# Optimization experiments

Hardware: AMD Instinct MI355X
Metric: run time of the kernel (lower is better)

## Reference

```python
import jax, jax.numpy as jnp
import numpy as np
from jax import lax

B, C_IN, C_OUT, KK, KS = 8, 32, 64, 4, 3
D, H, W = 32, 64, 64
PAD = 1

def setup_inputs() -> dict:
    key = jax.random.key(0)
    ks = jax.random.split(key, 12)
    s = 0.02
    return {
        "x": jax.random.normal(ks[0], (B, C_IN, D, H, W), jnp.float32),
        # K candidate conv kernels and biases
        "weight": jax.random.normal(ks[1], (KK, C_OUT, C_IN, KS, KS, KS), jnp.float32) * s,
        "cbias": jnp.zeros((KK, C_OUT), jnp.float32),
        "temperature": jnp.float32(34.0),
        # attention key path: BN(affine, eval-mode) -> GELU -> 1x1 conv (linear)
        "bn1_g": jnp.ones((C_IN,), jnp.float32),
        "bn1_b": jnp.zeros((C_IN,), jnp.float32),
        "w1": jax.random.normal(ks[2], (C_IN, C_IN), jnp.float32) * s,
        "b1": jnp.zeros((C_IN,), jnp.float32),
        "bn2_g": jnp.ones((C_IN,), jnp.float32),
        "bn2_b": jnp.zeros((C_IN,), jnp.float32),
        "w2": jax.random.normal(ks[3], (C_IN, C_IN), jnp.float32) * s,
        "b2": jnp.zeros((C_IN,), jnp.float32),
        "bn3_g": jnp.ones((C_IN,), jnp.float32),
        "bn3_b": jnp.zeros((C_IN,), jnp.float32),
        "w3": jax.random.normal(ks[4], (KK, C_IN), jnp.float32) * s,
        "b3": jnp.zeros((KK,), jnp.float32),
    }

def _attention(p, temperature, bn1_g, bn1_b, w1, b1, bn2_g, bn2_b, w2, b2, bn3_g, bn3_b, w3, b3):
    # p: [B, C] pooled features. 1x1x1 convs on 1x1x1 maps == linear layers.
    gelu = lambda t: jax.nn.gelu(t, approximate=False)  # torch nn.GELU default is erf
    a = gelu(p * bn1_g + bn1_b)          # BN (eval: rm=0, rv=1) + GELU
    a = a @ w1.T + b1
    a = gelu(a * bn2_g + bn2_b)
    a = a @ w2.T + b2
    a = a + p                            # ResidualLayer (plain add)
    a = a * bn3_g + bn3_b
    logits = a @ w3.T + b3               # [B, K]
    return jax.nn.softmax(logits / temperature, axis=1)

def reference(x, weight, cbias, temperature, bn1_g, bn1_b, w1, b1,
              bn2_g, bn2_b, w2, b2, bn3_g, bn3_b, w3, b3):
    # x: [B, C_in, D, H, W]
    p = x.mean(axis=(2, 3, 4))  # AdaptiveAvgPool3d(1)
    attn = _attention(p, temperature, bn1_g, bn1_b, w1, b1,
                      bn2_g, bn2_b, w2, b2, bn3_g, bn3_b, w3, b3)  # [B, K]
    # per-sample aggregated kernels / bias
    agg_w = jnp.einsum('bk,koidhw->boidhw', attn, weight)  # [B, O, I, k, k, k]
    agg_b = attn @ cbias                                    # [B, O]
    # grouped-conv trick (groups=B) == per-sample conv3d -> vmap over batch
    def conv1(xi, wi):
        return lax.conv_general_dilated(
            xi[None], wi, window_strides=(1, 1, 1),
            padding=[(PAD, PAD)] * 3,
            dimension_numbers=('NCDHW', 'OIDHW', 'NCDHW'))[0]
    out = jax.vmap(conv1)(x, agg_w)  # [B, O, D, H, W]
    return out + agg_b[:, :, None, None, None]
```

## Files before the change

kernel.cpp:

```cpp
#include <hip/hip_runtime.h>
#include <hip/hip_bf16.h>
#include <math.h>

#define B_   8
#define CIN  32
#define COUT 64
#define KK_  4
#define DD   32
#define HH   64
#define WW   64
#define HW   (HH*WW)
#define DHW  (DD*HH*WW)

typedef __attribute__((ext_vector_type(8)))  short bf16x8;
typedef __attribute__((ext_vector_type(16))) float f32x16;

__device__ __forceinline__ unsigned short f2bf(float f) {
    union { float f; unsigned int u; } v; v.f = f;
    return (unsigned short)((v.u + 0x7FFFu + ((v.u >> 16) & 1u)) >> 16);
}
__device__ __forceinline__ void gll16(const void* g, void* l) {
    __builtin_amdgcn_global_load_lds(
        (const __attribute__((address_space(1))) void*)g,
        (__attribute__((address_space(3))) void*)l, 16, 0, 0);
}

__global__ __launch_bounds__(256) void transpose_kernel(const float* __restrict__ x,
                                                        unsigned short* __restrict__ xt,
                                                        float* __restrict__ pblk) {
    const int t = threadIdx.x;
    const int r = t >> 6, w = t & 63;
    const int hb = blockIdx.x;
    const int h = (hb << 2) + r;
    const int d = blockIdx.y, b = blockIdx.z;

    const float* xb = x + (size_t)b*CIN*DHW + (size_t)d*HW + (size_t)h*WW + w;
    float f[CIN];
    #pragma unroll
    for (int c = 0; c < CIN; ++c) f[c] = xb[(size_t)c * DHW];

    unsigned int packed[CIN/2];
    #pragma unroll
    for (int c2 = 0; c2 < CIN/2; ++c2) {
        unsigned int lo = f2bf(f[2*c2]);
        unsigned int hi = f2bf(f[2*c2+1]);
        packed[c2] = lo | (hi << 16);
    }
    char* row = (char*)xt + (size_t)((b*DD + d)*HH + h) * 4096;
    #pragma unroll
    for (int q = 0; q < 4; ++q) {
        uint4 v = make_uint4(packed[4*q], packed[4*q+1], packed[4*q+2], packed[4*q+3]);
        *(uint4*)(row + q*1024 + (((w << 4)) ^ (q << 4))) = v;
    }

    #pragma unroll
    for (int off = 32; off > 0; off >>= 1) {
        #pragma unroll
        for (int c = 0; c < CIN; ++c) f[c] += __shfl_xor(f[c], off);
    }
    __shared__ float ws4[4][CIN];
    if ((t & 63) < CIN) ws4[r][t & 63] = f[t & 63];
    __syncthreads();
    if (t < CIN)
        pblk[(size_t)((b*DD + d)*16 + hb)*CIN + t] =
            ws4[0][t] + ws4[1][t] + ws4[2][t] + ws4[3][t];
}

__device__ __forceinline__ float gelu_erf(float v) {
    return 0.5f * v * (1.f + erff(v * 0.70710678118654752f));
}

__global__ void attn_kernel(const float* __restrict__ pblk,
                            const float* __restrict__ temperature,
                            const float* __restrict__ bn1_g, const float* __restrict__ bn1_b,
                            const float* __restrict__ w1,    const float* __restrict__ b1,
                            const float* __restrict__ bn2_g, const float* __restrict__ bn2_b,
                            const float* __restrict__ w2,    const float* __restrict__ b2,
                            const float* __restrict__ bn3_g, const float* __restrict__ bn3_b,
                            const float* __restrict__ w3,    const float* __restrict__ b3,
                            const float* __restrict__ cbias,
                            float* __restrict__ attn_out, float* __restrict__ aggb_out) {
    __shared__ float A[B_][CIN], A2[B_][CIN];
    __shared__ float L[B_][KK_], ATT[B_][KK_];
    const int t = threadIdx.x;
    const int b = t >> 5, c = t & 31;

    float pv = 0.f;
    for (int i = 0; i < DD*16; ++i) pv += pblk[(size_t)(b*DD*16 + i)*CIN + c];
    pv *= (1.f / (float)DHW);

    A[b][c] = gelu_erf(pv * bn1_g[c] + bn1_b[c]);
    __syncthreads();

    float s = b1[c];
    for (int j = 0; j < CIN; ++j) s += A[b][j] * w1[c*CIN + j];
    A2[b][c] = gelu_erf(s * bn2_g[c] + bn2_b[c]);
    __syncthreads();

    float s2 = b2[c];
    for (int j = 0; j < CIN; ++j) s2 += A2[b][j] * w2[c*CIN + j];
    s2 += pv;
    s2 = s2 * bn3_g[c] + bn3_b[c];
    __syncthreads();
    A[b][c] = s2;
    __syncthreads();

    if (c < KK_) {
        float lv = b3[c];
        for (int j = 0; j < CIN; ++j) lv += A[b][j] * w3[c*CIN + j];
        L[b][c] = lv;
    }
    __syncthreads();

    const float T = temperature[0];
    if (c < KK_) {
        float m = fmaxf(fmaxf(L[b][0], L[b][1]), fmaxf(L[b][2], L[b][3]));
        float e = expf((L[b][c] - m) / T);
        float den = 0.f;
        for (int j = 0; j < KK_; ++j) den += expf((L[b][j] - m) / T);
        float av = e / den;
        ATT[b][c] = av;
        attn_out[b*KK_ + c] = av;
    }
    __syncthreads();

    for (int o = c; o < COUT; o += CIN) {
        float sb = 0.f;
        for (int k = 0; k < KK_; ++k) sb += ATT[b][k] * cbias[k*COUT + o];
        aggb_out[b*COUT + o] = sb;
    }
}

__global__ void aggw_kernel(const float* __restrict__ weight,
                            const float* __restrict__ attn,
                            unsigned short* __restrict__ wt) {
    const int idx = blockIdx.x * 256 + threadIdx.x;
    const int ci   = idx & 31;
    const int co   = (idx >> 5) & 63;
    int r          = idx >> 11;
    const int kpos = r % 27;
    const int b    = r / 27;
    float s = 0.f;
    #pragma unroll
    for (int k = 0; k < KK_; ++k)
        s += attn[b*KK_ + k] * weight[((k*COUT + co)*CIN + ci)*27 + kpos];
    wt[idx] = f2bf(s);
}

__global__ __launch_bounds__(128, 1) void conv_mfma(const unsigned short* __restrict__ xt,
                                                    const unsigned short* __restrict__ wt,
                                                    const float* __restrict__ aggb,
                                                    float* __restrict__ out) {
    __shared__ char smem[19 * 4096];
    const int t    = threadIdx.x;
    const int lane = t & 63;
    const int wv   = t >> 6;
    const int lw   = lane & 31, lh = lane >> 5;

    const int id = blockIdx.x;
    const int b  = id & 7;
    const int h  = (id >> 3) & 63;
    const int d0 = ((id >> 9) & 7) << 2;

    const char* xb  = (const char*)xt + (size_t)(b*DD)*HH*4096;
    const char* wtb = (const char*)wt + (size_t)b * 27 * 4096;

    *(uint4*)&smem[18*4096 + t*32]      = make_uint4(0u,0u,0u,0u);
    *(uint4*)&smem[18*4096 + t*32 + 16] = make_uint4(0u,0u,0u,0u);

    for (int rid = wv; rid < 18; rid += 2) {
        const int j = rid / 3, ho = rid % 3;
        const int zd = d0 - 1 + j, yh = h - 1 + ho;
        char* dst = smem + (size_t)(rid << 12);
        if ((unsigned)zd < DD && (unsigned)yh < HH) {
            const char* src = xb + (size_t)(zd*HH + yh)*4096 + lane*16;
            #pragma unroll
            for (int q = 0; q < 4; ++q) gll16(src + (q << 10), dst + (q << 10));
        } else {
            #pragma unroll
            for (int q = 0; q < 4; ++q)
                *(uint4*)(dst + (q << 10) + lane*16) = make_uint4(0u,0u,0u,0u);
        }
    }
    __syncthreads();

    f32x16 acc[2][4];
    #pragma unroll
    for (int cb = 0; cb < 2; ++cb)
        #pragma unroll
        for (int r = 0; r < 4; ++r)
            acc[cb][r] = (f32x16){};

    const int a_off = lw*64 + lh*16;
    const int o0 = lh, o1 = 2 + lh;

    bf16x8 av[2][12];
    bf16x8 bc[2][12];

    auto loadA = [&](int p, int par) {
        const int kh = p / 3, kw = p % 3;
        #pragma unroll
        for (int kd = 0; kd < 3; ++kd) {
            const char* wk = wtb + (size_t)(((kd*3 + kh)*3 + kw) << 12);
            av[par][kd*4+0] = *(const bf16x8*)(wk + a_off);
            av[par][kd*4+1] = *(const bf16x8*)(wk + 32 + a_off);
            av[par][kd*4+2] = *(const bf16x8*)(wk + 2048 + a_off);
            av[par][kd*4+3] = *(const bf16x8*)(wk + 2048 + 32 + a_off);
        }
    };
    auto loadB = [&](int p, int par) {
        const int kh = p / 3, kw = p % 3;
        const int wp  = (wv << 5) + lw + kw - 1;
        const bool oob = ((unsigned)wp >= (unsigned)WW);
        const int wpc = oob ? lw : wp;
        const int sw0 = (o0 << 10) + ((wpc << 4) ^ (o0 << 4));
        const int sw1 = (o1 << 10) + ((wpc << 4) ^ (o1 << 4));
        #pragma unroll
        for (int j = 0; j < 6; ++j) {
            const int rb = oob ? 18*4096 : ((j*3 + kh) << 12);
            bc[par][j*2+0] = *(const bf16x8*)&smem[rb + sw0];
            bc[par][j*2+1] = *(const bf16x8*)&smem[rb + sw1];
        }
    };

    loadA(0, 0);
    loadB(0, 0);

    #pragma unroll
    for (int p = 0; p < 9; ++p) {
        const int cur = p & 1, nxt = cur ^ 1;
        if (p < 8) { loadA(p + 1, nxt); loadB(p + 1, nxt); }
        __builtin_amdgcn_sched_barrier(0);
        __builtin_amdgcn_s_setprio(1);
        #pragma unroll
        for (int kd = 0; kd < 3; ++kd) {
            #pragma unroll
            for (int r = 0; r < 4; ++r) {
                const int j = r + kd;
                acc[0][r] = __builtin_amdgcn_mfma_f32_32x32x16_bf16(av[cur][kd*4+0], bc[cur][j*2+0], acc[0][r], 0, 0, 0);
                acc[0][r] = __builtin_amdgcn_mfma_f32_32x32x16_bf16(av[cur][kd*4+1], bc[cur][j*2+1], acc[0][r], 0, 0, 0);
                acc[1][r] = __builtin_amdgcn_mfma_f32_32x32x16_bf16(av[cur][kd*4+2], bc[cur][j*2+0], acc[1][r], 0, 0, 0);
                acc[1][r] = __builtin_amdgcn_mfma_f32_32x32x16_bf16(av[cur][kd*4+3], bc[cur][j*2+1], acc[1][r], 0, 0, 0);
            }
        }
        __builtin_amdgcn_s_setprio(0);
    }

    const float* ab = aggb + b*COUT;
    const int sp0 = h*WW + (wv << 5) + lw;
    #pragma unroll
    for (int cb = 0; cb < 2; ++cb) {
        #pragma unroll
        for (int reg = 0; reg < 16; ++reg) {
            const int co = (cb << 5) + (reg & 3) + ((reg >> 2) << 3) + (lh << 2);
            const float bb = ab[co];
            float* oc = out + ((size_t)(b*COUT + co))*DHW + sp0;
            #pragma unroll
            for (int r = 0; r < 4; ++r)
                oc[(size_t)(d0 + r)*HW] = acc[cb][r][reg] + bb;
        }
    }
}

extern "C" void kernel_launch(void* const* d_in, const int* in_sizes, int n_in,
                              void* d_out, int out_size, void* d_ws, size_t ws_size,
                              hipStream_t stream) {
    const float* x           = (const float*)d_in[0];
    const float* weight      = (const float*)d_in[1];
    const float* cbias       = (const float*)d_in[2];
    const float* temperature = (const float*)d_in[3];
    const float* bn1_g       = (const float*)d_in[4];
    const float* bn1_b       = (const float*)d_in[5];
    const float* w1          = (const float*)d_in[6];
    const float* b1          = (const float*)d_in[7];
    const float* bn2_g       = (const float*)d_in[8];
    const float* bn2_b       = (const float*)d_in[9];
    const float* w2          = (const float*)d_in[10];
    const float* b2          = (const float*)d_in[11];
    const float* bn3_g       = (const float*)d_in[12];
    const float* bn3_b       = (const float*)d_in[13];
    const float* w3          = (const float*)d_in[14];
    const float* b3          = (const float*)d_in[15];
    float* out = (float*)d_out;

    char* ws = (char*)d_ws;
    float*          attn = (float*)(ws + 1024);
    float*          aggb = (float*)(ws + 4096);
    float*          pblk = (float*)(ws + 65536);
    unsigned short* wt   = (unsigned short*)(ws + 622592);
    unsigned short* xt   = (unsigned short*)(ws + 1507328);

    transpose_kernel<<<dim3(HH/4, DD, B_), 256, 0, stream>>>(x, xt, pblk);
    attn_kernel<<<1, 256, 0, stream>>>(pblk, temperature,
                                       bn1_g, bn1_b, w1, b1,
                                       bn2_g, bn2_b, w2, b2,
                                       bn3_g, bn3_b, w3, b3,
                                       cbias, attn, aggb);
    aggw_kernel<<<(B_*27*COUT*CIN)/256, 256, 0, stream>>>(weight, attn, wt);
    conv_mfma<<<dim3(64*8*8), 128, 0, stream>>>(xt, wt, aggb, out);
}
```

Measured before the change: 187.5 us.

## Split output channels across blocks and preload all weight fragments into registers

Each conv block now computes one half of the output channels, with the cv bit taken from the block index, which doubles the grid to 8192 blocks. Each block loads its 27 weight-position A fragments into registers once, overlapping the input LDS staging, instead of double-buffering them per kernel position. The aim is more parallelism and fewer per-iteration global loads of weights. In exchange, every input tile is staged into LDS twice (once per channel half), and the preloaded fragments raise register pressure.

```diff
diff --git a/kernel.cpp b/kernel.cpp
--- a/kernel.cpp
+++ b/kernel.cpp
@@ -159,11 +159,12 @@
 
     const int id = blockIdx.x;
     const int b  = id & 7;
-    const int h  = (id >> 3) & 63;
-    const int d0 = ((id >> 9) & 7) << 2;
+    const int cv = (id >> 3) & 1;
+    const int h  = (id >> 4) & 63;
+    const int d0 = ((id >> 10) & 7) << 2;
 
     const char* xb  = (const char*)xt + (size_t)(b*DD)*HH*4096;
-    const char* wtb = (const char*)wt + (size_t)b * 27 * 4096;
+    const char* wtb = (const char*)wt + (size_t)b * 27 * 4096 + (cv << 11);
 
     *(uint4*)&smem[18*4096 + t*32]      = make_uint4(0u,0u,0u,0u);
     *(uint4*)&smem[18*4096 + t*32 + 16] = make_uint4(0u,0u,0u,0u);
@@ -182,32 +183,25 @@
                 *(uint4*)(dst + (q << 10) + lane*16) = make_uint4(0u,0u,0u,0u);
         }
     }
-    __syncthreads();
-
-    f32x16 acc[2][4];
-    #pragma unroll
-    for (int cb = 0; cb < 2; ++cb)
-        #pragma unroll
-        for (int r = 0; r < 4; ++r)
-            acc[cb][r] = (f32x16){};
 
     const int a_off = lw*64 + lh*16;
+    bf16x8 avv[27][2];
+    #pragma unroll
+    for (int kp = 0; kp < 27; ++kp) {
+        const char* wk = wtb + (size_t)(kp << 12);
+        avv[kp][0] = *(const bf16x8*)(wk + a_off);
+        avv[kp][1] = *(const bf16x8*)(wk + 32 + a_off);
+    }
+
+    __syncthreads();
+
+    f32x16 acc[4];
+    #pragma unroll
+    for (int r = 0; r < 4; ++r) acc[r] = (f32x16){};
+
     const int o0 = lh, o1 = 2 + lh;
 
-    bf16x8 av[2][12];
-    bf16x8 bc[2][12];
-
-    auto loadA = [&](int p, int par) {
-        const int kh = p / 3, kw = p % 3;
-        #pragma unroll
-        for (int kd = 0; kd < 3; ++kd) {
-            const char* wk = wtb + (size_t)(((kd*3 + kh)*3 + kw) << 12);
-            av[par][kd*4+0] = *(const bf16x8*)(wk + a_off);
-            av[par][kd*4+1] = *(const bf16x8*)(wk + 32 + a_off);
-            av[par][kd*4+2] = *(const bf16x8*)(wk + 2048 + a_off);
-            av[par][kd*4+3] = *(const bf16x8*)(wk + 2048 + 32 + a_off);
-        }
-    };
+    bf16x8 bcp[2][12];
     auto loadB = [&](int p, int par) {
         const int kh = p / 3, kw = p % 3;
         const int wp  = (wv << 5) + lw + kw - 1;
@@ -218,29 +212,28 @@
         #pragma unroll
         for (int j = 0; j < 6; ++j) {
             const int rb = oob ? 18*4096 : ((j*3 + kh) << 12);
-            bc[par][j*2+0] = *(const bf16x8*)&smem[rb + sw0];
-            bc[par][j*2+1] = *(const bf16x8*)&smem[rb + sw1];
+            bcp[par][j*2+0] = *(const bf16x8*)&smem[rb + sw0];
+            bcp[par][j*2+1] = *(const bf16x8*)&smem[rb + sw1];
         }
     };
 
-    loadA(0, 0);
     loadB(0, 0);
 
     #pragma unroll
     for (int p = 0; p < 9; ++p) {
         const int cur = p & 1, nxt = cur ^ 1;
-        if (p < 8) { loadA(p + 1, nxt); loadB(p + 1, nxt); }
+        if (p < 8) loadB(p + 1, nxt);
         __builtin_amdgcn_sched_barrier(0);
+        const int kh = p / 3, kw = p % 3;
         __builtin_amdgcn_s_setprio(1);
         #pragma unroll
         for (int kd = 0; kd < 3; ++kd) {
+            const int kp = (kd*3 + kh)*3 + kw;
             #pragma unroll
             for (int r = 0; r < 4; ++r) {
                 const int j = r + kd;
-                acc[0][r] = __builtin_amdgcn_mfma_f32_32x32x16_bf16(av[cur][kd*4+0], bc[cur][j*2+0], acc[0][r], 0, 0, 0);
-                acc[0][r] = __builtin_amdgcn_mfma_f32_32x32x16_bf16(av[cur][kd*4+1], bc[cur][j*2+1], acc[0][r], 0, 0, 0);
-                acc[1][r] = __builtin_amdgcn_mfma_f32_32x32x16_bf16(av[cur][kd*4+2], bc[cur][j*2+0], acc[1][r], 0, 0, 0);
-                acc[1][r] = __builtin_amdgcn_mfma_f32_32x32x16_bf16(av[cur][kd*4+3], bc[cur][j*2+1], acc[1][r], 0, 0, 0);
+                acc[r] = __builtin_amdgcn_mfma_f32_32x32x16_bf16(avv[kp][0], bcp[cur][j*2+0], acc[r], 0, 0, 0);
+                acc[r] = __builtin_amdgcn_mfma_f32_32x32x16_bf16(avv[kp][1], bcp[cur][j*2+1], acc[r], 0, 0, 0);
             }
         }
         __builtin_amdgcn_s_setprio(0);
@@ -249,16 +242,13 @@
     const float* ab = aggb + b*COUT;
     const int sp0 = h*WW + (wv << 5) + lw;
     #pragma unroll
-    for (int cb = 0; cb < 2; ++cb) {
-        #pragma unroll
-        for (int reg = 0; reg < 16; ++reg) {
-            const int co = (cb << 5) + (reg & 3) + ((reg >> 2) << 3) + (lh << 2);
-            const float bb = ab[co];
-            float* oc = out + ((size_t)(b*COUT + co))*DHW + sp0;
-            #pragma unroll
-            for (int r = 0; r < 4; ++r)
-                oc[(size_t)(d0 + r)*HW] = acc[cb][r][reg] + bb;
-        }
+    for (int reg = 0; reg < 16; ++reg) {
+        const int co = (cv << 5) + (reg & 3) + ((reg >> 2) << 3) + (lh << 2);
+        const float bb = ab[co];
+        float* oc = out + ((size_t)(b*COUT + co))*DHW + sp0;
+        #pragma unroll
+        for (int r = 0; r < 4; ++r)
+            oc[(size_t)(d0 + r)*HW] = acc[r][reg] + bb;
     }
 }
 
@@ -297,5 +287,5 @@
                                        bn3_g, bn3_b, w3, b3,
                                        cbias, attn, aggb);
     aggw_kernel<<<(B_*27*COUT*CIN)/256, 256, 0, stream>>>(weight, attn, wt);
-    conv_mfma<<<dim3(64*8*8), 128, 0, stream>>>(xt, wt, aggb, out);
-}
+    conv_mfma<<<dim3(8192), 128, 0, stream>>>(xt, wt, aggb, out);
+}
```

Result: slower. 216.5 us (+15.5%).
